# Kernel optimization log

Hardware: AMD Instinct MI355X
Metric: run time of the kernel (lower is better)

Reference implementation:

```python
import jax, jax.numpy as jnp
import numpy as np
from jax import lax

N_QUBITS = 8
N_LAYERS = 7


def _conv(x, w, b, stride, pad):
    y = lax.conv_general_dilated(x, w, (stride, stride), [(pad, pad), (pad, pad)],
                                 dimension_numbers=('NCHW', 'OIHW', 'NCHW'))
    return y + b[None, :, None, None]


def _apply_1q(psi, M, q):
    # psi: (B, 2,2,...,2); apply 2x2 real matrix M on qubit q (axis q+1)
    a = q + 1
    pm = jnp.moveaxis(psi, a, 1)
    out = jnp.einsum('ij,bj...->bi...', M, pm)
    return jnp.moveaxis(out, 1, a)


def _apply_cnot(psi, c, t):
    ac, at = c + 1, t + 1
    pm = jnp.moveaxis(psi, (ac, at), (1, 2))
    top = pm[:, 0]
    bot = jnp.flip(pm[:, 1], axis=1)  # flip target when control=1
    pm = jnp.stack([top, bot], axis=1)
    return jnp.moveaxis(pm, (1, 2), (ac, at))


def _quantum(features, qw):
    psi = features / jnp.linalg.norm(features, axis=1, keepdims=True)
    B = psi.shape[0]
    psi = psi.reshape((B,) + (2,) * N_QUBITS)
    for l in range(N_LAYERS):
        for q in range(N_QUBITS):
            th = qw[l, q] / 2.0
            c, s = jnp.cos(th), jnp.sin(th)
            M = jnp.stack([jnp.stack([c, -s]), jnp.stack([s, c])])
            psi = _apply_1q(psi, M, q)
        for q in range(N_QUBITS - 1):
            psi = _apply_cnot(psi, q, q + 1)
    p = psi.reshape(B, 2, -1) ** 2
    return jnp.sum(p[:, 0], axis=1) - jnp.sum(p[:, 1], axis=1)  # <PauliZ(0)>


def setup_inputs() -> dict:
    key = jax.random.key(0)
    ks = jax.random.split(key, 20)
    def g(k, shape, fan_in):
        return jax.random.normal(k, shape, jnp.float32) * (1.0 / np.sqrt(fan_in))
    inp = {
        'x':  jax.random.normal(ks[0], (4096, 1, 64, 64), jnp.float32),
        'w1': g(ks[1], (4, 1, 5, 5), 25), 'b1': jnp.zeros((4,), jnp.float32),
        'w2': g(ks[2], (8, 4, 3, 3), 36), 'b2': jnp.zeros((8,), jnp.float32),
        'w3': g(ks[3], (16, 8, 3, 3), 72), 'b3': jnp.zeros((16,), jnp.float32),
        'wf': g(ks[4], (256, 64), 64), 'bf': jnp.zeros((256,), jnp.float32),
        'qw': jax.random.uniform(ks[5], (7, 8), jnp.float32, 0.0, 2 * np.pi),
        'wc1': g(ks[6], (200, 1), 1),   'bc1': jnp.zeros((200,), jnp.float32),
        'wc2': g(ks[7], (150, 200), 200), 'bc2': jnp.zeros((150,), jnp.float32),
        'wc3': g(ks[8], (100, 150), 150), 'bc3': jnp.zeros((100,), jnp.float32),
        'wc4': g(ks[9], (50, 100), 100),  'bc4': jnp.zeros((50,), jnp.float32),
        'wc5': g(ks[10], (1, 50), 50),    'bc5': jnp.zeros((1,), jnp.float32),
    }
    return inp


def reference(x, w1, b1, w2, b2, w3, b3, wf, bf, qw,
              wc1, bc1, wc2, bc2, wc3, bc3, wc4, bc4, wc5, bc5):
    # CNN feature extractor (dropout = identity at inference)
    h = jax.nn.relu(_conv(x, w1, b1, 2, 2))   # (B,4,32,32)
    h = jax.nn.relu(_conv(h, w2, b2, 2, 1))   # (B,8,16,16)
    h = jax.nn.relu(_conv(h, w3, b3, 1, 1))   # (B,16,16,16)
    B = h.shape[0]
    # AdaptiveAvgPool2d(2): 16x16 -> 2x2 via 8x8 non-overlapping means
    h = h.reshape(B, 16, 2, 8, 2, 8).mean(axis=(3, 5))  # (B,16,2,2)
    h = h.reshape(B, 64)
    feats = jax.nn.relu(h @ wf.T + bf)        # (B,256)
    # F.normalize(p=2, dim=1)
    feats = feats / jnp.maximum(jnp.linalg.norm(feats, axis=1, keepdims=True), 1e-12)
    # Batched 8-qubit statevector simulation (replaces per-sample Python loop)
    q = _quantum(feats, qw)[:, None]          # (B,1)
    # MLP classifier
    h = jax.nn.relu(q @ wc1.T + bc1)
    h = jax.nn.relu(h @ wc2.T + bc2)
    h = jax.nn.relu(h @ wc3.T + bc3)
    h = jax.nn.relu(h @ wc4.T + bc4)
    return jax.nn.sigmoid(h @ wc5.T + bc5)    # (B,1)
```

## Files before the change

kernel.cpp:

```cpp
#include <hip/hip_runtime.h>
#include <math.h>

typedef float v2f __attribute__((ext_vector_type(2)));
#define FMA2(a, b, c) __builtin_elementwise_fma((a), (b), (c))

__global__ __launch_bounds__(256, 6)
void convpool_kernel(const float* __restrict__ x,
                     const float* __restrict__ w1, const float* __restrict__ b1,
                     const float* __restrict__ w2, const float* __restrict__ b2,
                     const float* __restrict__ w3, const float* __restrict__ b3,
                     float* __restrict__ poolout)
{
    __shared__ __align__(16) float arena[4752];
    __shared__ __align__(16) float w3p[1552];
    const int tid  = threadIdx.x;
    const int b    = blockIdx.x;
    const int lane = tid & 63;

    for (int i = tid; i < 1152; i += 256) {
        int oc = i / 72, r = i - oc * 72;
        int ic = r / 9,  k = r - ic * 9;
        w3p[oc * 96 + ic * 12 + k] = w3[i];
    }
    if (tid < 16) w3p[1536 + tid] = b3[tid];
    for (int i = tid; i < 144; i += 256) { int oc = i / 36, c = i - oc * 36; arena[oc * 1188 + c] = 0.f; }
    for (int i = tid; i < 132; i += 256) { int oc = i / 33, r = i - oc * 33; arena[oc * 1188 + r * 36] = 0.f; }

    {
        const float* xb = x + (size_t)b * 4096;
        const int oh  = tid >> 3;
        const int ow  = tid & 7;
        const int ow0 = ow * 4;
        const int c0  = ow0 * 2 - 2;
        const bool cmL = (ow == 0);
        const bool cmR = (ow == 7);
        v2f a01[4], a23[4];
        #pragma unroll
        for (int oc = 0; oc < 4; oc++) {
            const float bv = b1[oc];
            a01[oc] = (v2f){bv, bv};
            a23[oc] = (v2f){bv, bv};
        }
        #pragma unroll
        for (int kh = 0; kh < 5; kh++) {
            const int ih = oh * 2 - 2 + kh;
            if (ih >= 0 && ih < 64) {
                const float* row = xb + ih * 64;
                float colv[11];
                {
                    float v0 = row[cmL ? 0 : c0];
                    float v1 = row[cmL ? 0 : c0 + 1];
                    float vA = row[cmR ? 63 : c0 + 10];
                    colv[0]  = cmL ? 0.f : v0;
                    colv[1]  = cmL ? 0.f : v1;
                    colv[10] = cmR ? 0.f : vA;
                }
                {
                    const float4 m0 = *(const float4*)(row + c0 + 2);
                    const float4 m1 = *(const float4*)(row + c0 + 6);
                    colv[2] = m0.x; colv[3] = m0.y; colv[4] = m0.z; colv[5] = m0.w;
                    colv[6] = m1.x; colv[7] = m1.y; colv[8] = m1.z; colv[9] = m1.w;
                }
                #pragma unroll
                for (int kw = 0; kw < 5; kw++) {
                    const v2f c01 = {colv[kw],     colv[kw + 2]};
                    const v2f c23 = {colv[kw + 4], colv[kw + 6]};
                    #pragma unroll
                    for (int oc = 0; oc < 4; oc++) {
                        const float wv = w1[oc * 25 + kh * 5 + kw];
                        const v2f ws = {wv, wv};
                        a01[oc] = FMA2(c01, ws, a01[oc]);
                        a23[oc] = FMA2(c23, ws, a23[oc]);
                    }
                }
            }
        }
        #pragma unroll
        for (int oc = 0; oc < 4; oc++) {
            float* o = arena + oc * 1188 + (oh + 1) * 36 + ow0 + 1;
            o[0] = fmaxf(a01[oc].x, 0.f); o[1] = fmaxf(a01[oc].y, 0.f);
            o[2] = fmaxf(a23[oc].x, 0.f); o[3] = fmaxf(a23[oc].y, 0.f);
        }
    }
    __syncthreads();

    v2f rA01, rA23, rB01, rB23;
    {
        const int oc0 = __builtin_amdgcn_readfirstlane(tid >> 6);
        const int oh  = lane >> 2, ow0 = (lane & 3) * 4;
        {
            const float ba = b2[oc0], bb = b2[oc0 + 4];
            rA01 = (v2f){ba, ba}; rA23 = (v2f){ba, ba};
            rB01 = (v2f){bb, bb}; rB23 = (v2f){bb, bb};
        }
        const int c0s = ow0 * 2;
        #pragma unroll
        for (int ic = 0; ic < 4; ic++) {
            const float* base = arena + ic * 1188;
            #pragma unroll
            for (int kh = 0; kh < 3; kh++) {
                const int ihs = oh * 2 + kh;
                const float* rp = base + ihs * 36 + c0s;
                const float4 q0 = *(const float4*)(rp);
                const float4 q1 = *(const float4*)(rp + 4);
                const float  q8 = rp[8];
                const float colv[9] = {q0.x, q0.y, q0.z, q0.w, q1.x, q1.y, q1.z, q1.w, q8};
                #pragma unroll
                for (int kw = 0; kw < 3; kw++) {
                    const v2f c01 = {colv[kw],     colv[kw + 2]};
                    const v2f c23 = {colv[kw + 4], colv[kw + 6]};
                    const float wa = w2[((oc0    ) * 4 + ic) * 9 + kh * 3 + kw];
                    const float wb = w2[((oc0 + 4) * 4 + ic) * 9 + kh * 3 + kw];
                    const v2f was = {wa, wa}, wbs = {wb, wb};
                    rA01 = FMA2(c01, was, rA01);
                    rA23 = FMA2(c23, was, rA23);
                    rB01 = FMA2(c01, wbs, rB01);
                    rB23 = FMA2(c23, wbs, rB23);
                }
            }
        }
    }
    __syncthreads();

    for (int i = tid; i < 544; i += 256) {
        const int ch = i / 68, j = i - ch * 68;
        if (j < 18)      arena[ch * 360 + j] = 0.f;
        else if (j < 36) arena[ch * 360 + 17 * 20 + (j - 18)] = 0.f;
        else if (j < 52) arena[ch * 360 + (j - 35) * 20] = 0.f;
        else             arena[ch * 360 + (j - 51) * 20 + 17] = 0.f;
    }
    {
        const int oc0 = __builtin_amdgcn_readfirstlane(tid >> 6);
        const int oh  = lane >> 2, ow0 = (lane & 3) * 4;
        float* oA = arena + oc0 * 360       + (oh + 1) * 20 + ow0 + 1;
        float* oB = arena + (oc0 + 4) * 360 + (oh + 1) * 20 + ow0 + 1;
        oA[0] = fmaxf(rA01.x, 0.f); oA[1] = fmaxf(rA01.y, 0.f);
        oA[2] = fmaxf(rA23.x, 0.f); oA[3] = fmaxf(rA23.y, 0.f);
        oB[0] = fmaxf(rB01.x, 0.f); oB[1] = fmaxf(rB01.y, 0.f);
        oB[2] = fmaxf(rB23.x, 0.f); oB[3] = fmaxf(rB23.y, 0.f);
    }
    __syncthreads();

    {
        const int oc = tid >> 4, s = tid & 15;
        const int tr = (s >> 2) * 4, tc = (s & 3) * 4;
        v2f acc2[4][2];
        const float bv = w3p[1536 + oc];
        #pragma unroll
        for (int r = 0; r < 4; r++) {
            acc2[r][0] = (v2f){bv, bv};
            acc2[r][1] = (v2f){bv, bv};
        }
        #pragma unroll
        for (int ic = 0; ic < 8; ic++) {
            const float* xc = arena + ic * 360;
            const float4 wv0 = *(const float4*)(w3p + oc * 96 + ic * 12);
            const float4 wv1 = *(const float4*)(w3p + oc * 96 + ic * 12 + 4);
            const float  wv8 = w3p[oc * 96 + ic * 12 + 8];
            const float wv[9] = {wv0.x, wv0.y, wv0.z, wv0.w, wv1.x, wv1.y, wv1.z, wv1.w, wv8};
            float p[6][6];
            #pragma unroll
            for (int dr = 0; dr < 6; dr++) {
                const float* rp = xc + (tr + dr) * 20 + tc;
                const float4 qa = *(const float4*)(rp);
                const float2 qb = *(const float2*)(rp + 4);
                p[dr][0] = qa.x; p[dr][1] = qa.y; p[dr][2] = qa.z;
                p[dr][3] = qa.w; p[dr][4] = qb.x; p[dr][5] = qb.y;
            }
            #pragma unroll
            for (int r = 0; r < 4; r++) {
                #pragma unroll
                for (int c2 = 0; c2 < 2; c2++) {
                    const int cb = c2 * 2;
                    v2f a = acc2[r][c2];
                    #pragma unroll
                    for (int kh = 0; kh < 3; kh++) {
                        #pragma unroll
                        for (int kw = 0; kw < 3; kw++) {
                            const v2f pp = {p[r + kh][cb + kw], p[r + kh][cb + kw + 1]};
                            const v2f ws = {wv[kh * 3 + kw], wv[kh * 3 + kw]};
                            a = FMA2(pp, ws, a);
                        }
                    }
                    acc2[r][c2] = a;
                }
            }
        }
        float ps = 0.f;
        #pragma unroll
        for (int r = 0; r < 4; r++) {
            ps += fmaxf(acc2[r][0].x, 0.f);
            ps += fmaxf(acc2[r][0].y, 0.f);
            ps += fmaxf(acc2[r][1].x, 0.f);
            ps += fmaxf(acc2[r][1].y, 0.f);
        }
        ps += __shfl_xor(ps, 1, 64);
        ps += __shfl_xor(ps, 4, 64);
        if ((s & 5) == 0) {
            const int ii = s >> 3, jj = (s >> 1) & 1;
            poolout[b * 64 + oc * 4 + ii * 2 + jj] = ps * (1.f / 64.f);
        }
    }
}

__global__ __launch_bounds__(256)
void head_kernel(const float* __restrict__ poolin,
                 const float* __restrict__ wf, const float* __restrict__ bf,
                 const float* __restrict__ qw,
                 const float* __restrict__ wc1, const float* __restrict__ bc1,
                 const float* __restrict__ wc2, const float* __restrict__ bc2,
                 const float* __restrict__ wc3, const float* __restrict__ bc3,
                 const float* __restrict__ wc4, const float* __restrict__ bc4,
                 const float* __restrict__ wc5, const float* __restrict__ bc5,
                 float* __restrict__ out)
{
    __shared__ __align__(16) float pool_s[256];
    __shared__ __align__(16) float feats[1024];
    __shared__ __align__(16) float h1[800];
    __shared__ __align__(16) float h2[600];
    __shared__ __align__(16) float h3[400];
    __shared__ __align__(16) float h4[200];
    __shared__ float zbuf[4];
    __shared__ float csc[56], css[56];

    const int tid  = threadIdx.x;
    const int blk  = blockIdx.x;
    const int lane = tid & 63;
    const int wv   = tid >> 6;

    pool_s[tid] = poolin[(size_t)blk * 256 + tid];
    if (tid < 56) {
        float th = qw[tid] * 0.5f;
        csc[tid] = cosf(th);
        css[tid] = sinf(th);
    }
    __syncthreads();

    {
        float acc[4];
        const float bv = bf[tid];
        #pragma unroll
        for (int e = 0; e < 4; e++) acc[e] = bv;
        const float4* wr = (const float4*)(wf + tid * 64);
        #pragma unroll
        for (int kc = 0; kc < 4; kc++) {
            float4 w0 = wr[kc * 4 + 0], w1_ = wr[kc * 4 + 1], w2_ = wr[kc * 4 + 2], w3_ = wr[kc * 4 + 3];
            #pragma unroll
            for (int e = 0; e < 4; e++) {
                const float4* pp = (const float4*)(pool_s + e * 64 + kc * 16);
                float4 p0 = pp[0], p1 = pp[1], p2 = pp[2], p3 = pp[3];
                float a = acc[e];
                a = fmaf(w0.x, p0.x, a); a = fmaf(w0.y, p0.y, a); a = fmaf(w0.z, p0.z, a); a = fmaf(w0.w, p0.w, a);
                a = fmaf(w1_.x, p1.x, a); a = fmaf(w1_.y, p1.y, a); a = fmaf(w1_.z, p1.z, a); a = fmaf(w1_.w, p1.w, a);
                a = fmaf(w2_.x, p2.x, a); a = fmaf(w2_.y, p2.y, a); a = fmaf(w2_.z, p2.z, a); a = fmaf(w2_.w, p2.w, a);
                a = fmaf(w3_.x, p3.x, a); a = fmaf(w3_.y, p3.y, a); a = fmaf(w3_.z, p3.z, a); a = fmaf(w3_.w, p3.w, a);
                acc[e] = a;
            }
        }
        #pragma unroll
        for (int e = 0; e < 4; e++) feats[e * 256 + tid] = fmaxf(acc[e], 0.f);
    }
    __syncthreads();

    {
        const float* base = feats + wv * 256;
        float v0 = base[lane], v1 = base[64 + lane];
        float v2 = base[128 + lane], v3 = base[192 + lane];
        float ssq = v0 * v0 + v1 * v1 + v2 * v2 + v3 * v3;
        #pragma unroll
        for (int off = 1; off < 64; off <<= 1) ssq += __shfl_xor(ssq, off, 64);
        const float inv = 1.0f / fmaxf(sqrtf(ssq), 1e-12f);
        v0 *= inv; v1 *= inv; v2 *= inv; v3 *= inv;

        for (int l = 0; l < 7; l++) {
            {
                float c = csc[l * 8 + 0], s = css[l * 8 + 0];
                float n0 = c * v0 - s * v2, n2 = s * v0 + c * v2;
                float n1 = c * v1 - s * v3, n3 = s * v1 + c * v3;
                float c1 = csc[l * 8 + 1], s1 = css[l * 8 + 1];
                v0 = c1 * n0 - s1 * n1; v1 = s1 * n0 + c1 * n1;
                v2 = c1 * n2 - s1 * n3; v3 = s1 * n2 + c1 * n3;
            }
            #pragma unroll
            for (int q = 2; q < 8; q++) {
                const int m = 1 << (7 - q);
                const float c = csc[l * 8 + q], s = css[l * 8 + q];
                const float sgn = (lane & m) ? s : -s;
                float t0 = __shfl_xor(v0, m, 64);
                float t1 = __shfl_xor(v1, m, 64);
                float t2 = __shfl_xor(v2, m, 64);
                float t3 = __shfl_xor(v3, m, 64);
                v0 = fmaf(sgn, t0, c * v0);
                v1 = fmaf(sgn, t1, c * v1);
                v2 = fmaf(sgn, t2, c * v2);
                v3 = fmaf(sgn, t3, c * v3);
            }
            { float t = v2; v2 = v3; v3 = t; }
            v1 = __shfl_xor(v1, 32, 64);
            v3 = __shfl_xor(v3, 32, 64);
            #pragma unroll
            for (int q = 2; q < 7; q++) {
                const int mc = 1 << (7 - q), mt = 1 << (6 - q);
                float t0 = __shfl_xor(v0, mt, 64);
                float t1 = __shfl_xor(v1, mt, 64);
                float t2 = __shfl_xor(v2, mt, 64);
                float t3 = __shfl_xor(v3, mt, 64);
                if (lane & mc) { v0 = t0; v1 = t1; v2 = t2; v3 = t3; }
            }
        }
        float m0 = v0 * v0 + v1 * v1 - v2 * v2 - v3 * v3;
        #pragma unroll
        for (int off = 1; off < 64; off <<= 1) m0 += __shfl_xor(m0, off, 64);
        if (lane == 0) zbuf[wv] = m0;
    }
    __syncthreads();

    if (tid < 200) {
        const float w = wc1[tid], bv = bc1[tid];
        #pragma unroll
        for (int e = 0; e < 4; e++) h1[e * 200 + tid] = fmaxf(fmaf(zbuf[e], w, bv), 0.f);
    }
    __syncthreads();
    if (tid < 150) {
        float acc[4];
        const float bv = bc2[tid];
        #pragma unroll
        for (int e = 0; e < 4; e++) acc[e] = bv;
        const float4* wr = (const float4*)(wc2 + tid * 200);
        for (int kc = 0; kc < 25; kc++) {
            float4 wa = wr[2 * kc], wb = wr[2 * kc + 1];
            #pragma unroll
            for (int e = 0; e < 4; e++) {
                const float4* hp = (const float4*)(h1 + e * 200) + 2 * kc;
                float4 ha = hp[0], hb = hp[1];
                float a = acc[e];
                a = fmaf(wa.x, ha.x, a); a = fmaf(wa.y, ha.y, a); a = fmaf(wa.z, ha.z, a); a = fmaf(wa.w, ha.w, a);
                a = fmaf(wb.x, hb.x, a); a = fmaf(wb.y, hb.y, a); a = fmaf(wb.z, hb.z, a); a = fmaf(wb.w, hb.w, a);
                acc[e] = a;
            }
        }
        #pragma unroll
        for (int e = 0; e < 4; e++) h2[e * 150 + tid] = fmaxf(acc[e], 0.f);
    }
    __syncthreads();
    if (tid < 100) {
        float acc[4];
        const float bv = bc3[tid];
        #pragma unroll
        for (int e = 0; e < 4; e++) acc[e] = bv;
        const float2* wr = (const float2*)(wc3 + tid * 150);
        for (int k = 0; k < 75; k++) {
            float2 wa = wr[k];
            #pragma unroll
            for (int e = 0; e < 4; e++) {
                float2 hv = ((const float2*)(h2 + e * 150))[k];
                acc[e] = fmaf(wa.x, hv.x, fmaf(wa.y, hv.y, acc[e]));
            }
        }
        #pragma unroll
        for (int e = 0; e < 4; e++) h3[e * 100 + tid] = fmaxf(acc[e], 0.f);
    }
    __syncthreads();
    if (tid < 50) {
        float acc[4];
        const float bv = bc4[tid];
        #pragma unroll
        for (int e = 0; e < 4; e++) acc[e] = bv;
        const float4* wr = (const float4*)(wc4 + tid * 100);
        for (int kc = 0; kc < 25; kc++) {
            float4 wa = wr[kc];
            #pragma unroll
            for (int e = 0; e < 4; e++) {
                float4 hv = ((const float4*)(h3 + e * 100))[kc];
                float a = acc[e];
                a = fmaf(wa.x, hv.x, a); a = fmaf(wa.y, hv.y, a);
                a = fmaf(wa.z, hv.z, a); a = fmaf(wa.w, hv.w, a);
                acc[e] = a;
            }
        }
        #pragma unroll
        for (int e = 0; e < 4; e++) h4[e * 50 + tid] = fmaxf(acc[e], 0.f);
    }
    __syncthreads();
    if (tid < 4) {
        float acc = bc5[0];
        const float2* wr = (const float2*)wc5;
        #pragma unroll
        for (int k = 0; k < 25; k++) {
            float2 wa = wr[k];
            float2 hv = ((const float2*)(h4 + tid * 50))[k];
            acc = fmaf(wa.x, hv.x, fmaf(wa.y, hv.y, acc));
        }
        out[blk * 4 + tid] = 1.0f / (1.0f + expf(-acc));
    }
}

extern "C" void kernel_launch(void* const* d_in, const int* in_sizes, int n_in,
                              void* d_out, int out_size, void* d_ws, size_t ws_size,
                              hipStream_t stream) {
    const float* x   = (const float*)d_in[0];
    const float* w1  = (const float*)d_in[1];
    const float* b1  = (const float*)d_in[2];
    const float* w2  = (const float*)d_in[3];
    const float* b2  = (const float*)d_in[4];
    const float* w3  = (const float*)d_in[5];
    const float* b3  = (const float*)d_in[6];
    const float* wf  = (const float*)d_in[7];
    const float* bf  = (const float*)d_in[8];
    const float* qw  = (const float*)d_in[9];
    const float* wc1 = (const float*)d_in[10];
    const float* bc1 = (const float*)d_in[11];
    const float* wc2 = (const float*)d_in[12];
    const float* bc2 = (const float*)d_in[13];
    const float* wc3 = (const float*)d_in[14];
    const float* bc3 = (const float*)d_in[15];
    const float* wc4 = (const float*)d_in[16];
    const float* bc4 = (const float*)d_in[17];
    const float* wc5 = (const float*)d_in[18];
    const float* bc5 = (const float*)d_in[19];
    float* out = (float*)d_out;

    float* poolbuf = (float*)d_ws;

    convpool_kernel<<<4096, 256, 0, stream>>>(x, w1, b1, w2, b2, w3, b3, poolbuf);
    head_kernel<<<1024, 256, 0, stream>>>(poolbuf, wf, bf, qw,
                                          wc1, bc1, wc2, bc2, wc3, bc3,
                                          wc4, bc4, wc5, bc5, out);
}
```

Measured before the change: 222.6 us.

## Shrink LDS footprint, swizzle conv1 output, stage conv3 weights via registers

Removes the separate w3 shared buffer: conv3 weights are loaded into registers at kernel start and written into the reused arena after conv2, cutting LDS per block so more blocks (launch bound raised from 6 to 8) can be resident. Conv1 output is stored unpadded with float4 stores and an XOR block swizzle to avoid bank conflicts, and conv2 handles the padding borders in-register. This adds index arithmetic and register pressure from holding six weight values across the first two stages, which could cause spills under the tighter bound.

```diff
diff --git a/kernel.cpp b/kernel.cpp
--- a/kernel.cpp
+++ b/kernel.cpp
@@ -4,27 +4,29 @@
 typedef float v2f __attribute__((ext_vector_type(2)));
 #define FMA2(a, b, c) __builtin_elementwise_fma((a), (b), (c))
 
-__global__ __launch_bounds__(256, 6)
+__global__ __launch_bounds__(256, 8)
 void convpool_kernel(const float* __restrict__ x,
                      const float* __restrict__ w1, const float* __restrict__ b1,
                      const float* __restrict__ w2, const float* __restrict__ b2,
                      const float* __restrict__ w3, const float* __restrict__ b3,
                      float* __restrict__ poolout)
 {
-    __shared__ __align__(16) float arena[4752];
-    __shared__ __align__(16) float w3p[1552];
+    __shared__ __align__(16) float arena[4608];
     const int tid  = threadIdx.x;
     const int b    = blockIdx.x;
     const int lane = tid & 63;
 
-    for (int i = tid; i < 1152; i += 256) {
-        int oc = i / 72, r = i - oc * 72;
-        int ic = r / 9,  k = r - ic * 9;
-        w3p[oc * 96 + ic * 12 + k] = w3[i];
-    }
-    if (tid < 16) w3p[1536 + tid] = b3[tid];
-    for (int i = tid; i < 144; i += 256) { int oc = i / 36, c = i - oc * 36; arena[oc * 1188 + c] = 0.f; }
-    for (int i = tid; i < 132; i += 256) { int oc = i / 33, r = i - oc * 33; arena[oc * 1188 + r * 36] = 0.f; }
+    float wstage[6];
+    #pragma unroll
+    for (int j = 0; j < 6; j++) {
+        const int s  = tid + 256 * j;
+        const int oc = s / 96;
+        const int r  = s - oc * 96;
+        const int ic = r / 12;
+        const int k  = r - ic * 12;
+        wstage[j] = (k < 9) ? w3[oc * 72 + ic * 9 + k] : 0.f;
+    }
+    const float bstage = (tid < 16) ? b3[tid] : 0.f;
 
     {
         const float* xb = x + (size_t)b * 4096;
@@ -75,11 +77,13 @@
                 }
             }
         }
+        const int bsw1 = (oh >> 1) & 1;
         #pragma unroll
         for (int oc = 0; oc < 4; oc++) {
-            float* o = arena + oc * 1188 + (oh + 1) * 36 + ow0 + 1;
-            o[0] = fmaxf(a01[oc].x, 0.f); o[1] = fmaxf(a01[oc].y, 0.f);
-            o[2] = fmaxf(a23[oc].x, 0.f); o[3] = fmaxf(a23[oc].y, 0.f);
+            float4 v;
+            v.x = fmaxf(a01[oc].x, 0.f); v.y = fmaxf(a01[oc].y, 0.f);
+            v.z = fmaxf(a23[oc].x, 0.f); v.w = fmaxf(a23[oc].y, 0.f);
+            *(float4*)(arena + oc * 1152 + oh * 36 + ((ow ^ bsw1) << 2)) = v;
         }
     }
     __syncthreads();
@@ -87,24 +91,35 @@
     v2f rA01, rA23, rB01, rB23;
     {
         const int oc0 = __builtin_amdgcn_readfirstlane(tid >> 6);
-        const int oh  = lane >> 2, ow0 = (lane & 3) * 4;
+        const int oh  = lane >> 2;
+        const int w   = lane & 3;
         {
             const float ba = b2[oc0], bb = b2[oc0 + 4];
             rA01 = (v2f){ba, ba}; rA23 = (v2f){ba, ba};
             rB01 = (v2f){bb, bb}; rB23 = (v2f){bb, bb};
         }
-        const int c0s = ow0 * 2;
         #pragma unroll
         for (int ic = 0; ic < 4; ic++) {
-            const float* base = arena + ic * 1188;
+            const float* base = arena + ic * 1152;
             #pragma unroll
             for (int kh = 0; kh < 3; kh++) {
-                const int ihs = oh * 2 + kh;
-                const float* rp = base + ihs * 36 + c0s;
-                const float4 q0 = *(const float4*)(rp);
-                const float4 q1 = *(const float4*)(rp + 4);
-                const float  q8 = rp[8];
-                const float colv[9] = {q0.x, q0.y, q0.z, q0.w, q1.x, q1.y, q1.z, q1.w, q8};
+                const int r2 = 2 * oh + kh - 1;
+                const int rc = (kh == 0) ? ((oh == 0) ? 0 : r2) : r2;
+                const int bsw = (rc >> 1) & 1;
+                const float* row = base + rc * 36;
+                const float4 qA = *(const float4*)(row + (((2 * w)     ^ bsw) << 2));
+                const float4 qB = *(const float4*)(row + (((2 * w + 1) ^ bsw) << 2));
+                const int sblk = (w == 0) ? bsw : ((2 * w - 1) ^ bsw);
+                const float sv = row[(sblk << 2) + 3];
+                float colv[9];
+                colv[0] = (w == 0) ? 0.f : sv;
+                colv[1] = qA.x; colv[2] = qA.y; colv[3] = qA.z; colv[4] = qA.w;
+                colv[5] = qB.x; colv[6] = qB.y; colv[7] = qB.z; colv[8] = qB.w;
+                if (kh == 0) {
+                    const bool rvalid = (oh > 0);
+                    #pragma unroll
+                    for (int t = 0; t < 9; t++) colv[t] = rvalid ? colv[t] : 0.f;
+                }
                 #pragma unroll
                 for (int kw = 0; kw < 3; kw++) {
                     const v2f c01 = {colv[kw],     colv[kw + 2]};
@@ -139,13 +154,19 @@
         oB[0] = fmaxf(rB01.x, 0.f); oB[1] = fmaxf(rB01.y, 0.f);
         oB[2] = fmaxf(rB23.x, 0.f); oB[3] = fmaxf(rB23.y, 0.f);
     }
-    __syncthreads();
-
-    {
+    #pragma unroll
+    for (int j = 0; j < 6; j++) {
+        arena[2880 + tid + 256 * j] = wstage[j];
+    }
+    if (tid < 16) arena[4416 + tid] = bstage;
+    __syncthreads();
+
+    {
+        const float* w3s = arena + 2880;
         const int oc = tid >> 4, s = tid & 15;
         const int tr = (s >> 2) * 4, tc = (s & 3) * 4;
         v2f acc2[4][2];
-        const float bv = w3p[1536 + oc];
+        const float bv = w3s[1536 + oc];
         #pragma unroll
         for (int r = 0; r < 4; r++) {
             acc2[r][0] = (v2f){bv, bv};
@@ -154,9 +175,9 @@
         #pragma unroll
         for (int ic = 0; ic < 8; ic++) {
             const float* xc = arena + ic * 360;
-            const float4 wv0 = *(const float4*)(w3p + oc * 96 + ic * 12);
-            const float4 wv1 = *(const float4*)(w3p + oc * 96 + ic * 12 + 4);
-            const float  wv8 = w3p[oc * 96 + ic * 12 + 8];
+            const float4 wv0 = *(const float4*)(w3s + oc * 96 + ic * 12);
+            const float4 wv1 = *(const float4*)(w3s + oc * 96 + ic * 12 + 4);
+            const float  wv8 = w3s[oc * 96 + ic * 12 + 8];
             const float wv[9] = {wv0.x, wv0.y, wv0.z, wv0.w, wv1.x, wv1.y, wv1.z, wv1.w, wv8};
             float p[6][6];
             #pragma unroll
```

Result: faster. 215.5 us (-3.2%).
